# Kernel tuning notes

Hardware: AMD Instinct MI355X
Metric: run time of the kernel (lower is better)

## Reference

```python
import jax, jax.numpy as jnp
import numpy as np

BN_EPS = 1e-5

def _sqdist(a, b):
    # a: (B,N,3), b: (B,M,3) -> (B,N,M)
    return (jnp.sum(a**2, -1)[:, :, None] + jnp.sum(b**2, -1)[:, None, :]
            - 2.0 * jnp.einsum('bnc,bmc->bnm', a, b))

def _knn_idx(pts, k):
    # smallest-k neighbor indices, (B,N,k)
    d = _sqdist(pts, pts)
    _, idx = jax.lax.top_k(-d, k)
    return idx

def _group(feat, idx):
    # feat (B,C,N), idx (B,N,K) -> (B,C,N,K)
    return jax.vmap(lambda f, i: f[:, i])(feat, idx)

def _gather_pts(pts, idx):
    # pts (B,M,C), idx (B,...) -> (B,...,C)
    return jax.vmap(lambda p, i: p[i])(pts, idx)

def _conv1(w, b, x):
    # 1x1 conv1d: w (O,C), x (B,C,N)
    return jnp.einsum('oc,bcn->bon', w, x) + b[None, :, None]

def _conv2(w, x, b=None):
    # 1x1 conv2d: w (O,C), x (B,C,N,K)
    y = jnp.einsum('oc,bcnk->bonk', w, x)
    return y if b is None else y + b[None, :, None, None]

def _bn_eval(x, gamma, beta):
    # eval-mode BatchNorm2d with running_mean=0, running_var=1
    s = gamma / jnp.sqrt(1.0 + BN_EPS)
    return x * s[None, :, None, None] + beta[None, :, None, None]

def _lgrp(x_q, x, P_anchor, map_idx, anchor_dist, lw1, lw2, lw3, k=16):
    # x_q, x: (B,n,3) -> weights (B,dim,n,k)
    d = _sqdist(x_q, x)
    _, idx = jax.lax.top_k(-d, k)                      # (B,n,k)
    neighbors = _gather_pts(x, idx)                    # (B,n,k,3)
    R1 = jnp.abs(x_q[:, :, None, :] - neighbors)       # (B,n,k,3)
    B_idx = _gather_pts(map_idx[..., None], idx)[..., 0]  # (B,n,k)
    anchorA = _gather_pts(P_anchor, map_idx)           # (B,n,3)
    anchorB = _gather_pts(P_anchor, B_idx)             # (B,n,k,3)
    dA = jnp.linalg.norm(x_q - anchorA, axis=-1)       # (B,n)
    dB = jnp.linalg.norm(neighbors - anchorB, axis=-1) # (B,n,k)
    dAB = jax.vmap(lambda ad, a, bi: ad[a[:, None], bi])(anchor_dist, map_idx, B_idx)
    R2s = dA[:, :, None] + dAB + dB                    # (B,n,k)
    R2 = jnp.broadcast_to(R2s[..., None], R1.shape)
    feats = jnp.concatenate([R1, R2], axis=-1).transpose(0, 3, 1, 2)  # (B,6,n,k)
    h = jax.nn.relu(_conv2(lw1, feats))
    h = jax.nn.relu(_conv2(lw2, h))
    return _conv2(lw3, h)                              # (B,dim,n,k)

def setup_inputs() -> dict:
    key = jax.random.key(0)
    ks = jax.random.split(key, 32)
    B, C_in, n, dim, M, k = 2, 128, 2048, 256, 128, 16
    hid_p, hid_a = 64, dim * 4
    s = 0.05
    inp = {
        'x': jax.random.normal(ks[0], (B, C_in, n), jnp.float32),
        'pos': jax.random.normal(ks[1], (B, 3, n), jnp.float32),
        'fps_idx': jax.random.randint(ks[2], (B, n), 0, n),
        'P_anchor': jax.random.normal(ks[3], (B, M, 3), jnp.float32),
        'map_idx': jax.random.randint(ks[4], (B, n), 0, M),
        'anchor_dist': jax.random.uniform(ks[5], (B, M, M), jnp.float32) * 2.0,
        'w_start': jax.random.normal(ks[6], (dim, C_in)) * s,
        'b_start': jnp.zeros((dim,), jnp.float32),
        'w_key': jax.random.normal(ks[7], (dim, dim)) * s,
        'b_key': jnp.zeros((dim,), jnp.float32),
        'w_query': jax.random.normal(ks[8], (dim, dim)) * s,
        'b_query': jnp.zeros((dim,), jnp.float32),
        'w_value': jax.random.normal(ks[9], (dim, dim)) * s,
        'b_value': jnp.zeros((dim,), jnp.float32),
        'pw1': jax.random.normal(ks[10], (hid_p, 3)) * s,
        'pb1': jnp.zeros((hid_p,), jnp.float32),
        'pg1': jnp.ones((hid_p,), jnp.float32),
        'pbt1': jnp.zeros((hid_p,), jnp.float32),
        'pw2': jax.random.normal(ks[11], (dim, hid_p)) * s,
        'pb2': jnp.zeros((dim,), jnp.float32),
        'lw1': jax.random.normal(ks[12], (32, 6)) * s,
        'lw2': jax.random.normal(ks[13], (64, 32)) * s,
        'lw3': jax.random.normal(ks[14], (dim, 64)) * s,
        'aw1': jax.random.normal(ks[15], (hid_a, dim)) * s,
        'ab1': jnp.zeros((hid_a,), jnp.float32),
        'ag1': jnp.ones((hid_a,), jnp.float32),
        'abt1': jnp.zeros((hid_a,), jnp.float32),
        'aw2': jax.random.normal(ks[16], (dim, hid_a)) * s,
        'ab2': jnp.zeros((dim,), jnp.float32),
        'w_end': jax.random.normal(ks[17], (C_in, dim)) * s,
        'b_end': jnp.zeros((C_in,), jnp.float32),
    }
    return inp

def reference(x, pos, fps_idx, P_anchor, map_idx, anchor_dist,
              w_start, b_start, w_key, b_key, w_query, b_query, w_value, b_value,
              pw1, pb1, pg1, pbt1, pw2, pb2, lw1, lw2, lw3,
              aw1, ab1, ag1, abt1, aw2, ab2, w_end, b_end):
    n_knn = 16
    identity = x
    xf = _conv1(w_start, b_start, x)                   # (B,dim,n)
    pos_f = pos.transpose(0, 2, 1)                     # (B,n,3)
    idx_knn = _knn_idx(pos_f, n_knn)                   # (B,n,k)
    key_f = _conv1(w_key, b_key, xf)
    value = _conv1(w_value, b_value, xf)
    query = _conv1(w_query, b_query, xf)
    key_g = _group(key_f, idx_knn)                     # (B,dim,n,k)
    qk_rel = query[:, :, :, None] - key_g
    pos_rel = pos[:, :, :, None] - _group(pos, idx_knn)
    f_l = _lgrp(pos_f, pos_f, P_anchor, map_idx, anchor_dist, lw1, lw2, lw3, k=16)
    # pos_mlp: conv-bn-relu-conv
    h = _bn_eval(_conv2(pw1, pos_rel, pb1), pg1, pbt1)
    pos_emb = _conv2(pw2, jax.nn.relu(h), pb2)         # (B,dim,n,k)
    # attn_mlp
    a = _bn_eval(_conv2(aw1, qk_rel + pos_emb + f_l, ab1), ag1, abt1)
    attention = _conv2(aw2, jax.nn.relu(a), ab2)
    attention = jax.nn.softmax(attention, axis=-1)
    value_e = value[:, :, :, None] + pos_emb + f_l
    agg = jnp.sum(attention * value_e, axis=-1)        # (B,dim,n)
    y = _conv1(w_end, b_end, agg)
    return y + identity
```

## Files before the change

kernel.cpp:

```cpp
#include <hip/hip_runtime.h>
#include <hip/hip_bf16.h>

typedef __hip_bfloat16 bf16;
typedef unsigned short u16;
typedef __attribute__((ext_vector_type(8))) short s8v;
typedef __attribute__((ext_vector_type(4))) float f32x4;

#define NP    2048
#define DC    256
#define MA    128
#define KNN_  16
#define LKV   768

#define MFMA_B16(a,b,c) __builtin_amdgcn_mfma_f32_16x16x32_bf16(a,b,c,0,0,0)

__device__ __forceinline__ float u2f(u16 u){ return __uint_as_float(((unsigned int)u)<<16); }
__device__ __forceinline__ u16 f2u(float f){ bf16 h=__float2bfloat16(f); u16 us; __builtin_memcpy(&us,&h,2); return us; }

__device__ __forceinline__ s8v ldpk(const u16* pk, int rb, int KS, int ks, int l){
  return *(const s8v*)(pk + (((size_t)((rb*KS + ks)*64 + l))<<3));
}
__device__ __forceinline__ s8v ldsB(const u16* base, int col, int k0, int rshift){
  int byte = ((col<<rshift) + (k0<<1)) ^ ((col&7)<<4);
  return *(const s8v*)((const char*)base + byte);
}
__device__ __forceinline__ void st2(u16* base, int col, int ch0, int rshift,
                                    float v0, float v1, float v2, float v3){
  uint2 pkv;
  pkv.x = (unsigned)f2u(v0) | ((unsigned)f2u(v1)<<16);
  pkv.y = (unsigned)f2u(v2) | ((unsigned)f2u(v3)<<16);
  int byte = ((col<<rshift) + (ch0<<1)) ^ ((col&7)<<4);
  *(uint2*)((char*)base + byte) = pkv;
}
__device__ __forceinline__ void st1(u16* base, int col, int ch, int rshift, float v){
  int byte = ((col<<rshift) + (ch<<1)) ^ ((col&7)<<4);
  *(u16*)((char*)base + byte) = f2u(v);
}
__device__ __forceinline__ void ld4s(const u16* base, int col, int ch0, int rshift, float* o){
  int byte = ((col<<rshift) + (ch0<<1)) ^ ((col&7)<<4);
  uint2 pkv = *(const uint2*)((const char*)base + byte);
  o[0] = u2f(pkv.x & 0xffff); o[1] = u2f(pkv.x>>16);
  o[2] = u2f(pkv.y & 0xffff); o[3] = u2f(pkv.y>>16);
}

template<bool XT, bool OT, bool RES>
__global__ __launch_bounds__(256) void mgemm(
    const u16* __restrict__ apk, const float* __restrict__ X,
    const float* __restrict__ bias, const float* __restrict__ resid,
    float* __restrict__ out, int M, int N, int K, int ldo)
{
  __shared__ u16 Bt[64*256];
  const int tid = threadIdx.x;
  const int w = tid>>6, l = tid&63, k = l&15, g = l>>4;
  const int n0 = blockIdx.x*64, m0 = blockIdx.y*128, bb = blockIdx.z;
  const int KS = K >> 5;
  if constexpr (!XT) {
    for (int e = tid*4; e < 64*K; e += 1024) {
      int kk = e >> 6, c = e & 63;
      float4 v = *(const float4*)(X + (size_t)bb*K*N + (size_t)kk*N + n0 + c);
      st1(Bt, c+0, kk, 9, v.x); st1(Bt, c+1, kk, 9, v.y);
      st1(Bt, c+2, kk, 9, v.z); st1(Bt, c+3, kk, 9, v.w);
    }
  } else {
    for (int e = tid*4; e < 64*256; e += 1024) {
      int c = e >> 8, kk = e & 255;
      float4 v = *(const float4*)(X + ((size_t)bb*N + n0 + c)*256 + kk);
      st2(Bt, c, kk, 9, v.x, v.y, v.z, v.w);
    }
  }
  __syncthreads();
  f32x4 acc[2][4] = {};
  const int rbase = (m0>>4) + w*2;
  for (int ks = 0; ks < KS; ks++) {
    s8v a0 = ldpk(apk, rbase,   KS, ks, l);
    s8v a1 = ldpk(apk, rbase+1, KS, ks, l);
#pragma unroll
    for (int cf = 0; cf < 4; cf++) {
      s8v bF = ldsB(Bt, cf*16 + k, ks*32 + g*8, 9);
      acc[0][cf] = MFMA_B16(a0, bF, acc[0][cf]);
      acc[1][cf] = MFMA_B16(a1, bF, acc[1][cf]);
    }
  }
#pragma unroll
  for (int ri = 0; ri < 2; ri++) {
    int mrow = m0 + w*32 + ri*16 + g*4;
#pragma unroll
    for (int r = 0; r < 4; r++) {
      int m = mrow + r;
      float bv = bias[m];
#pragma unroll
      for (int cf = 0; cf < 4; cf++) {
        int n = n0 + cf*16 + k;
        float v = acc[ri][cf][r] + bv;
        if constexpr (RES) v += resid[((size_t)bb*M + m)*N + n];
        if constexpr (OT) out[((size_t)bb*N + n)*ldo + m] = v;
        else              out[((size_t)bb*M + m)*N + n] = v;
      }
    }
  }
}

__global__ __launch_bounds__(1024) void knn_kernel(const float* __restrict__ pos, int* __restrict__ idx)
{
  __shared__ float px[NP], py[NP], pz[NP], pn[NP];
  const int tid = threadIdx.x;
  const int w = tid >> 6, l = tid & 63;
  const int bb = blockIdx.x >> 7;
  const int q0 = (blockIdx.x & 127) * 16;
  const float* pp = pos + (size_t)bb * 3 * NP;
  for (int t = tid; t < NP; t += 1024) {
    float x = pp[t], y = pp[NP + t], z = pp[2*NP + t];
    px[t] = x; py[t] = y; pz[t] = z; pn[t] = x*x + y*y + z*z;
  }
  __syncthreads();
  const int qi = q0 + w;
  const float qx = px[qi], qy = py[qi], qz = pz[qi], qn = pn[qi];
  float bd[16]; int bi[16];
#pragma unroll
  for (int t = 0; t < 16; t++) { bd[t] = 3.4e38f; bi[t] = -1; }
  float worst = 3.4e38f;
  for (int t = 0; t < 32; t++) {
    int j = t*64 + l;
    float d = qn + pn[j] - 2.f * (qx*px[j] + qy*py[j] + qz*pz[j]);
    if (__any(d < worst)) {
      float cd = (d < worst) ? d : 3.4e38f;
      int   cj = j;
#pragma unroll
      for (int s = 0; s < 16; s++) {
        bool sw = cd < bd[s];
        float od = bd[s]; int oj = bi[s];
        bd[s] = sw ? cd : od;  bi[s] = sw ? cj : oj;
        cd    = sw ? od : cd;  cj    = sw ? oj : cj;
      }
      worst = bd[15];
    }
  }
  int myj = 0;
#pragma unroll
  for (int r = 0; r < 16; r++) {
    float md = bd[0]; int mj = bi[0];
#pragma unroll
    for (int o = 1; o < 64; o <<= 1) {
      float od = __shfl_xor(md, o);
      int   oj = __shfl_xor(mj, o);
      bool tk = (od < md) || (od == md && ((unsigned)oj < (unsigned)mj));
      md = tk ? od : md;  mj = tk ? oj : mj;
    }
    if (l == r) myj = mj;
    bool win = (bi[0] == mj);
#pragma unroll
    for (int s = 0; s < 15; s++) {
      bd[s] = win ? bd[s+1] : bd[s];
      bi[s] = win ? bi[s+1] : bi[s];
    }
    bd[15] = win ? 3.4e38f : bd[15];
  }
  if (l < 16) idx[((size_t)bb * NP + qi) * KNN_ + l] = myj;
}

__global__ __launch_bounds__(256) void prep_kernel(
    const float* __restrict__ aw1, const float* __restrict__ aw2,
    const float* __restrict__ lw3, const float* __restrict__ pw2,
    const float* __restrict__ w_start, const float* __restrict__ w_key,
    const float* __restrict__ w_query, const float* __restrict__ w_value,
    const float* __restrict__ w_end,
    const float* __restrict__ b_key, const float* __restrict__ b_query,
    const float* __restrict__ b_value,
    const float* __restrict__ ag1, const float* __restrict__ ab1, const float* __restrict__ abt1,
    const float* __restrict__ pg1, const float* __restrict__ pb1, const float* __restrict__ pbt1,
    u16* __restrict__ aw1pk, u16* __restrict__ aw2pk, u16* __restrict__ wppk,
    u16* __restrict__ wstpk, u16* __restrict__ wkqvpk, u16* __restrict__ wendpk,
    float* __restrict__ sa, float* __restrict__ oa, float* __restrict__ sp,
    float* __restrict__ op_, float* __restrict__ bkqv)
{
  int i = blockIdx.x * 256 + threadIdx.x;
  const float inv = rsqrtf(1.0f + 1e-5f);
  if (i < 262144) {
    int rb = i >> 12, rem = i & 4095, ks = rem >> 9, l = (rem >> 3) & 63, j = rem & 7;
    int row = rb*16 + (l & 15), colk = ks*32 + (l >> 4)*8 + j;
    aw1pk[i] = f2u(aw1[(size_t)row*256 + colk]); return;
  }
  i -= 262144;
  if (i < 262144) {
    int rb = i >> 14, rem = i & 16383, ks = rem >> 9, l = (rem >> 3) & 63, j = rem & 7;
    int row = rb*16 + (l & 15), colk = ks*32 + (l >> 4)*8 + j;
    aw2pk[i] = f2u(aw2[(size_t)row*1024 + colk]); return;
  }
  i -= 262144;
  if (i < 32768) {
    int rb = i >> 11, rem = i & 2047, ks = rem >> 9, l = (rem >> 3) & 63, j = rem & 7;
    int row = rb*16 + (l & 15), colk = ks*32 + (l >> 4)*8 + j;
    float v = (colk < 64) ? lw3[row*64 + colk] : pw2[row*64 + (colk - 64)];
    wppk[i] = f2u(v); return;
  }
  i -= 32768;
  if (i < 32768) {
    int rb = i >> 11, rem = i & 2047, ks = rem >> 9, l = (rem >> 3) & 63, j = rem & 7;
    int row = rb*16 + (l & 15), colk = ks*32 + (l >> 4)*8 + j;
    wstpk[i] = f2u(w_start[(size_t)row*128 + colk]); return;
  }
  i -= 32768;
  if (i < 196608) {
    int rb = i >> 12, rem = i & 4095, ks = rem >> 9, l = (rem >> 3) & 63, j = rem & 7;
    int row = rb*16 + (l & 15), colk = ks*32 + (l >> 4)*8 + j;
    float v = (row < 256) ? w_key[(size_t)row*256 + colk]
            : (row < 512) ? w_query[(size_t)(row-256)*256 + colk]
                          : w_value[(size_t)(row-512)*256 + colk];
    wkqvpk[i] = f2u(v); return;
  }
  i -= 196608;
  if (i < 32768) {
    int rb = i >> 12, rem = i & 4095, ks = rem >> 9, l = (rem >> 3) & 63, j = rem & 7;
    int row = rb*16 + (l & 15), colk = ks*32 + (l >> 4)*8 + j;
    wendpk[i] = f2u(w_end[(size_t)row*256 + colk]); return;
  }
  i -= 32768;
  if (i < 1024) { float s_ = ag1[i]*inv; sa[i] = s_; oa[i] = ab1[i]*s_ + abt1[i]; return; }
  i -= 1024;
  if (i < 64)  { float s_ = pg1[i]*inv; sp[i] = s_; op_[i] = pb1[i]*s_ + pbt1[i]; return; }
  i -= 64;
  if (i < 768) {
    bkqv[i] = (i < 256) ? b_key[i] : (i < 512) ? b_query[i-256] : b_value[i-512];
  }
}

__global__ __launch_bounds__(256, 2) void fused_attn(
    const float* __restrict__ kqv, const int* __restrict__ knn_idx,
    const float* __restrict__ pos, const int* __restrict__ map_idx,
    const float* __restrict__ P_anchor, const float* __restrict__ adist,
    const float* __restrict__ lw1f, const float* __restrict__ lw2f, const float* __restrict__ pw1f,
    const float* __restrict__ spv, const float* __restrict__ opv, const float* __restrict__ pb2f,
    const u16* __restrict__ aw1pk, const float* __restrict__ sav, const float* __restrict__ oav,
    const u16* __restrict__ aw2pk, const u16* __restrict__ wppk, const float* __restrict__ ab2f,
    float* __restrict__ aggT)
{
  __shared__ __align__(16) char smem[40960];
  u16*   s_t   = (u16*)smem;
  u16*   hid_t = (u16*)(smem + 32768);
  float* fFEAT = (float*)smem;
  float* fPREL = (float*)(smem + 1632);
  u16*   fH1   = (u16*) (smem + 2448);

  const int tid = threadIdx.x;
  const int w = tid >> 6, l = tid & 63;
  const int k = l & 15, g = l >> 4;
  const int p0 = blockIdx.x * 4;
  const int b = p0 >> 11, pi0 = p0 & 2047;
  const int pi = pi0 + w;
  const int col_w = w*16 + k;

  const float* kqvB = kqv + (size_t)b * NP * LKV;
  const int* knnB = knn_idx + ((size_t)b * NP) * KNN_;

  if (l < 16) {
    int kk = l;
    int j = knnB[(size_t)pi * KNN_ + kk];
    const float* pp = pos + (size_t)b * 3 * NP;
    float qx = pp[pi], qy = pp[NP+pi], qz = pp[2*NP+pi];
    float nx = pp[j],  ny = pp[NP+j],  nz = pp[2*NP+j];
    float r1x = qx-nx, r1y = qy-ny, r1z = qz-nz;
    fPREL[(w*3+0)*17+kk] = r1x; fPREL[(w*3+1)*17+kk] = r1y; fPREL[(w*3+2)*17+kk] = r1z;
    int mi = map_idx[b*NP + pi];
    int bj = map_idx[b*NP + j];
    const float* pa = P_anchor + (size_t)b * MA * 3;
    float ax = pa[mi*3], ay = pa[mi*3+1], az = pa[mi*3+2];
    float bx = pa[bj*3], by = pa[bj*3+1], bz = pa[bj*3+2];
    float dA = sqrtf((qx-ax)*(qx-ax)+(qy-ay)*(qy-ay)+(qz-az)*(qz-az));
    float dB = sqrtf((nx-bx)*(nx-bx)+(ny-by)*(ny-by)+(nz-bz)*(nz-bz));
    float dAB = adist[(size_t)b*MA*MA + mi*MA + bj];
    float r2 = dA + dAB + dB;
    fFEAT[(w*6+0)*17+kk] = fabsf(r1x); fFEAT[(w*6+1)*17+kk] = fabsf(r1y);
    fFEAT[(w*6+2)*17+kk] = fabsf(r1z);
    fFEAT[(w*6+3)*17+kk] = r2; fFEAT[(w*6+4)*17+kk] = r2; fFEAT[(w*6+5)*17+kk] = r2;
  }
  __syncthreads();

  {
    float f0=fFEAT[(w*6+0)*17+k], f1=fFEAT[(w*6+1)*17+k], f2=fFEAT[(w*6+2)*17+k],
          f3=fFEAT[(w*6+3)*17+k], f4=fFEAT[(w*6+4)*17+k], f5=fFEAT[(w*6+5)*17+k];
#pragma unroll
    for (int jj = 0; jj < 8; jj++) {
      int h = g*8 + jj;
      const float* wp = lw1f + h*6;
      float v = wp[0]*f0 + wp[1]*f1 + wp[2]*f2 + wp[3]*f3 + wp[4]*f4 + wp[5]*f5;
      fH1[(w*32+h)*17+k] = f2u(fmaxf(v, 0.f));
    }
  }
  __syncthreads();

  {
    float hr[32];
#pragma unroll
    for (int t = 0; t < 32; t++) hr[t] = u2f(fH1[(w*32+t)*17+k]);
#pragma unroll
    for (int jj = 0; jj < 16; jj++) {
      int h = g*16 + jj;
      const float4* wp = (const float4*)(lw2f + h*32);
      float a = 0.f;
#pragma unroll
      for (int t4 = 0; t4 < 8; t4++) {
        float4 wv = wp[t4];
        a += wv.x*hr[t4*4] + wv.y*hr[t4*4+1] + wv.z*hr[t4*4+2] + wv.w*hr[t4*4+3];
      }
      st1(hid_t, col_w, h, 7, fmaxf(a, 0.f));
    }
  }
  __syncthreads();

  f32x4 accs[4][4];
  {
#pragma unroll
    for (int fr = 0; fr < 4; fr++) {
      int ch0 = w*64 + fr*16 + g*4;
      const float4 p4 = *(const float4*)(pb2f + ch0);
#pragma unroll
      for (int fc = 0; fc < 4; fc++) {
        int j = knnB[(size_t)(pi0 + fc) * KNN_ + k];
        const float4 q4 = *(const float4*)(kqvB + (size_t)(pi0 + fc)*LKV + 256 + ch0);
        const float4 k4 = *(const float4*)(kqvB + (size_t)j*LKV + ch0);
        accs[fr][fc][0] = q4.x - k4.x + p4.x;
        accs[fr][fc][1] = q4.y - k4.y + p4.y;
        accs[fr][fc][2] = q4.z - k4.z + p4.z;
        accs[fr][fc][3] = q4.w - k4.w + p4.w;
      }
    }
#pragma unroll
    for (int ks = 0; ks < 2; ks++) {
      s8v aF[4];
#pragma unroll
      for (int fr = 0; fr < 4; fr++) aF[fr] = ldpk(wppk, w*4 + fr, 4, ks, l);
#pragma unroll
      for (int fc = 0; fc < 4; fc++) {
        s8v bF = ldsB(hid_t, fc*16 + k, ks*32 + g*8, 7);
#pragma unroll
        for (int fr = 0; fr < 4; fr++) accs[fr][fc] = MFMA_B16(aF[fr], bF, accs[fr][fc]);
      }
    }
  }
  __syncthreads();

  {
    float pr0 = fPREL[(w*3+0)*17+k], pr1 = fPREL[(w*3+1)*17+k], pr2 = fPREL[(w*3+2)*17+k];
#pragma unroll
    for (int jj = 0; jj < 16; jj++) {
      int h = g*16 + jj;
      float d = pw1f[h*3]*pr0 + pw1f[h*3+1]*pr1 + pw1f[h*3+2]*pr2;
      st1(hid_t, col_w, h, 7, fmaxf(d*spv[h] + opv[h], 0.f));
    }
  }
  __syncthreads();

  {
#pragma unroll
    for (int ks = 0; ks < 2; ks++) {
      s8v aF[4];
#pragma unroll
      for (int fr = 0; fr < 4; fr++) aF[fr] = ldpk(wppk, w*4 + fr, 4, 2 + ks, l);
#pragma unroll
      for (int fc = 0; fc < 4; fc++) {
        s8v bF = ldsB(hid_t, fc*16 + k, ks*32 + g*8, 7);
#pragma unroll
        for (int fr = 0; fr < 4; fr++) accs[fr][fc] = MFMA_B16(aF[fr], bF, accs[fr][fc]);
      }
    }
#pragma unroll
    for (int fr = 0; fr < 4; fr++)
#pragma unroll
      for (int fc = 0; fc < 4; fc++)
        st2(s_t, fc*16 + k, w*64 + fr*16 + g*4, 9,
            accs[fr][fc][0], accs[fr][fc][1], accs[fr][fc][2], accs[fr][fc][3]);
  }
  __syncthreads();

  f32x4 acc2[4][4];
#pragma unroll
  for (int fr = 0; fr < 4; fr++) {
    const float4 a4 = *(const float4*)(ab2f + w*64 + fr*16 + g*4);
#pragma unroll
    for (int fc = 0; fc < 4; fc++) {
      acc2[fr][fc][0] = a4.x; acc2[fr][fc][1] = a4.y;
      acc2[fr][fc][2] = a4.z; acc2[fr][fc][3] = a4.w;
    }
  }

  for (int c = 0; c < 16; c++) {
    f32x4 acc1[4] = {};
    const int rb = c*4 + w;
#pragma unroll
    for (int ks = 0; ks < 8; ks++) {
      s8v a0 = ldpk(aw1pk, rb, 8, ks, l);
#pragma unroll
      for (int cf = 0; cf < 4; cf++) {
        s8v bF = ldsB(s_t, cf*16 + k, ks*32 + g*8, 9);
        acc1[cf] = MFMA_B16(a0, bF, acc1[cf]);
      }
    }
    __syncthreads();
    {
      int hl = w*16 + g*4;
      int hg = rb*16 + g*4;
      const float4 sc = *(const float4*)(sav + hg);
      const float4 of = *(const float4*)(oav + hg);
#pragma unroll
      for (int cf = 0; cf < 4; cf++) {
        float v0 = fmaxf(acc1[cf][0]*sc.x + of.x, 0.f);
        float v1 = fmaxf(acc1[cf][1]*sc.y + of.y, 0.f);
        float v2 = fmaxf(acc1[cf][2]*sc.z + of.z, 0.f);
        float v3 = fmaxf(acc1[cf][3]*sc.w + of.w, 0.f);
        st2(hid_t, cf*16 + k, hl, 7, v0, v1, v2, v3);
      }
    }
    __syncthreads();
#pragma unroll
    for (int ks = 0; ks < 2; ks++) {
      s8v aF[4];
#pragma unroll
      for (int rf = 0; rf < 4; rf++) aF[rf] = ldpk(aw2pk, w*4 + rf, 32, c*2 + ks, l);
#pragma unroll
      for (int cf = 0; cf < 4; cf++) {
        s8v bF = ldsB(hid_t, cf*16 + k, ks*32 + g*8, 7);
#pragma unroll
        for (int rf = 0; rf < 4; rf++) acc2[rf][cf] = MFMA_B16(aF[rf], bF, acc2[rf][cf]);
      }
    }
  }

#pragma unroll
  for (int fc = 0; fc < 4; fc++) {
    int j = knnB[(size_t)(pi0 + fc) * KNN_ + k];
    const float* qp = kqvB + (size_t)(pi0 + fc)*LKV + 256;
    const float* kp = kqvB + (size_t)j*LKV;
    const float* vp = kqvB + (size_t)(pi0 + fc)*LKV + 512;
#pragma unroll
    for (int fr = 0; fr < 4; fr++) {
      int ch0 = w*64 + fr*16 + g*4;
      float q4[4], k4[4], v4[4], s4[4], res[4];
      *(float4*)q4 = *(const float4*)(qp + ch0);
      *(float4*)k4 = *(const float4*)(kp + ch0);
      *(float4*)v4 = *(const float4*)(vp + ch0);
      ld4s(s_t, fc*16 + k, ch0, 9, s4);
#pragma unroll
      for (int r = 0; r < 4; r++) {
        float a = acc2[fr][fc][r];
        float m = a;
        m = fmaxf(m, __shfl_xor(m, 1, 16)); m = fmaxf(m, __shfl_xor(m, 2, 16));
        m = fmaxf(m, __shfl_xor(m, 4, 16)); m = fmaxf(m, __shfl_xor(m, 8, 16));
        float ex = __expf(a - m);
        float se = ex;
        se += __shfl_xor(se, 1, 16); se += __shfl_xor(se, 2, 16);
        se += __shfl_xor(se, 4, 16); se += __shfl_xor(se, 8, 16);
        float watt = ex / se;
        float ve = v4[r] - q4[r] + k4[r] + s4[r];
        float cc = watt * ve;
        cc += __shfl_xor(cc, 1, 16); cc += __shfl_xor(cc, 2, 16);
        cc += __shfl_xor(cc, 4, 16); cc += __shfl_xor(cc, 8, 16);
        res[r] = cc;
      }
      if (k == 0)
        *(float4*)(aggT + ((size_t)(b*NP) + pi0 + fc)*DC + ch0) =
            make_float4(res[0], res[1], res[2], res[3]);
    }
  }
}

extern "C" void kernel_launch(void* const* d_in, const int* in_sizes, int n_in,
                              void* d_out, int out_size, void* d_ws, size_t ws_size,
                              hipStream_t stream)
{
  const float* x        = (const float*)d_in[0];
  const float* pos      = (const float*)d_in[1];
  const float* P_anchor = (const float*)d_in[3];
  const int*   map_idx  = (const int*)  d_in[4];
  const float* adist    = (const float*)d_in[5];
  const float* w_start  = (const float*)d_in[6];
  const float* b_start  = (const float*)d_in[7];
  const float* w_key    = (const float*)d_in[8];
  const float* b_key    = (const float*)d_in[9];
  const float* w_query  = (const float*)d_in[10];
  const float* b_query  = (const float*)d_in[11];
  const float* w_value  = (const float*)d_in[12];
  const float* b_value  = (const float*)d_in[13];
  const float* pw1      = (const float*)d_in[14];
  const float* pb1      = (const float*)d_in[15];
  const float* pg1      = (const float*)d_in[16];
  const float* pbt1     = (const float*)d_in[17];
  const float* pw2      = (const float*)d_in[18];
  const float* pb2      = (const float*)d_in[19];
  const float* lw1      = (const float*)d_in[20];
  const float* lw2      = (const float*)d_in[21];
  const float* lw3      = (const float*)d_in[22];
  const float* aw1      = (const float*)d_in[23];
  const float* ab1      = (const float*)d_in[24];
  const float* ag1      = (const float*)d_in[25];
  const float* abt1     = (const float*)d_in[26];
  const float* aw2      = (const float*)d_in[27];
  const float* ab2      = (const float*)d_in[28];
  const float* w_end    = (const float*)d_in[29];
  const float* b_end    = (const float*)d_in[30];

  if (ws_size < (size_t)4672384 * 4) return;

  float* ws     = (float*)d_ws;
  float* xf     = ws + 0;
  float* aggT   = ws + 0;
  float* kqvT   = ws + 1048576;
  u16*   aw1pk  = (u16*)(ws + 4194304);
  u16*   aw2pk  = (u16*)(ws + 4325376);
  u16*   wppk   = (u16*)(ws + 4456448);
  u16*   wstpk  = (u16*)(ws + 4472832);
  u16*   wkqvpk = (u16*)(ws + 4489216);
  u16*   wendpk = (u16*)(ws + 4587520);
  float* sa     = ws + 4603904;
  float* oa     = ws + 4604928;
  float* sp     = ws + 4605952;
  float* op_    = ws + 4606016;
  float* bkqv   = ws + 4606080;
  int*   knn_i  = (int*)(ws + 4606848);

  prep_kernel<<<3208, 256, 0, stream>>>(aw1, aw2, lw3, pw2,
      w_start, w_key, w_query, w_value, w_end, b_key, b_query, b_value,
      ag1, ab1, abt1, pg1, pb1, pbt1,
      aw1pk, aw2pk, wppk, wstpk, wkqvpk, wendpk, sa, oa, sp, op_, bkqv);

  mgemm<false, false, false><<<dim3(32, 2, 2), 256, 0, stream>>>(
      wstpk, x, b_start, nullptr, xf, 256, NP, 128, 0);

  knn_kernel<<<256, 1024, 0, stream>>>(pos, knn_i);

  mgemm<false, true, false><<<dim3(32, 6, 2), 256, 0, stream>>>(
      wkqvpk, xf, bkqv, nullptr, kqvT, 768, NP, 256, LKV);

  fused_attn<<<1024, 256, 0, stream>>>(kqvT, knn_i,
      pos, map_idx, P_anchor, adist,
      lw1, lw2, pw1, sp, op_, pb2,
      aw1pk, sa, oa, aw2pk, wppk, ab2, aggT);

  mgemm<true, false, true><<<dim3(32, 1, 2), 256, 0, stream>>>(
      wendpk, aggT, b_end, x, (float*)d_out, 128, NP, 256, 0);
}
```

Measured before the change: 234.8 us.

## Use 8 waves per block in fused attention, halving per-wave channel tiles

The fused attention kernel now runs 512 threads (8 waves) per block instead of 256. Each wave owns 32 output channels instead of 64, which halves the per-wave MFMA accumulator arrays. The lw2 and pos_mlp hidden computations now run in one phase and write into a single 128-wide hidden buffer, so the two pos_emb GEMM passes merge into one K=128 pass. This targets more latency hiding and lower register pressure per wave. The costs are more LDS per block (48KB), an extra barrier, and the larger block must still fit within the new launch bounds.

```diff
diff --git a/kernel.cpp b/kernel.cpp
--- a/kernel.cpp
+++ b/kernel.cpp
@@ -224,7 +224,7 @@
   }
 }
 
-__global__ __launch_bounds__(256, 2) void fused_attn(
+__global__ __launch_bounds__(512, 4) void fused_attn(
     const float* __restrict__ kqv, const int* __restrict__ knn_idx,
     const float* __restrict__ pos, const int* __restrict__ map_idx,
     const float* __restrict__ P_anchor, const float* __restrict__ adist,
@@ -234,7 +234,7 @@
     const u16* __restrict__ aw2pk, const u16* __restrict__ wppk, const float* __restrict__ ab2f,
     float* __restrict__ aggT)
 {
-  __shared__ __align__(16) char smem[40960];
+  __shared__ __align__(16) char smem[49152];
   u16*   s_t   = (u16*)smem;
   u16*   hid_t = (u16*)(smem + 32768);
   float* fFEAT = (float*)smem;
@@ -246,14 +246,13 @@
   const int k = l & 15, g = l >> 4;
   const int p0 = blockIdx.x * 4;
   const int b = p0 >> 11, pi0 = p0 & 2047;
-  const int pi = pi0 + w;
-  const int col_w = w*16 + k;
 
   const float* kqvB = kqv + (size_t)b * NP * LKV;
   const int* knnB = knn_idx + ((size_t)b * NP) * KNN_;
 
-  if (l < 16) {
+  if (w < 4 && l < 16) {
     int kk = l;
+    int pi = pi0 + w;
     int j = knnB[(size_t)pi * KNN_ + kk];
     const float* pp = pos + (size_t)b * 3 * NP;
     float qx = pp[pi], qy = pp[NP+pi], qz = pp[2*NP+pi];
@@ -275,7 +274,7 @@
   }
   __syncthreads();
 
-  {
+  if (w < 4) {
     float f0=fFEAT[(w*6+0)*17+k], f1=fFEAT[(w*6+1)*17+k], f2=fFEAT[(w*6+2)*17+k],
           f3=fFEAT[(w*6+3)*17+k], f4=fFEAT[(w*6+4)*17+k], f5=fFEAT[(w*6+5)*17+k];
 #pragma unroll
@@ -289,12 +288,14 @@
   __syncthreads();
 
   {
+    const int p = w & 3, hh = w >> 2;
+    const int col_p = p*16 + k;
     float hr[32];
 #pragma unroll
-    for (int t = 0; t < 32; t++) hr[t] = u2f(fH1[(w*32+t)*17+k]);
-#pragma unroll
-    for (int jj = 0; jj < 16; jj++) {
-      int h = g*16 + jj;
+    for (int t = 0; t < 32; t++) hr[t] = u2f(fH1[(p*32+t)*17+k]);
+#pragma unroll
+    for (int jj = 0; jj < 8; jj++) {
+      int h = hh*32 + g*8 + jj;
       const float4* wp = (const float4*)(lw2f + h*32);
       float a = 0.f;
 #pragma unroll
@@ -302,16 +303,23 @@
         float4 wv = wp[t4];
         a += wv.x*hr[t4*4] + wv.y*hr[t4*4+1] + wv.z*hr[t4*4+2] + wv.w*hr[t4*4+3];
       }
-      st1(hid_t, col_w, h, 7, fmaxf(a, 0.f));
+      st1(hid_t, col_p, h, 8, fmaxf(a, 0.f));
+    }
+    float pr0 = fPREL[(p*3+0)*17+k], pr1 = fPREL[(p*3+1)*17+k], pr2 = fPREL[(p*3+2)*17+k];
+#pragma unroll
+    for (int jj = 0; jj < 8; jj++) {
+      int h = hh*32 + g*8 + jj;
+      float d = pw1f[h*3]*pr0 + pw1f[h*3+1]*pr1 + pw1f[h*3+2]*pr2;
+      st1(hid_t, col_p, 64 + h, 8, fmaxf(d*spv[h] + opv[h], 0.f));
     }
   }
   __syncthreads();
 
-  f32x4 accs[4][4];
   {
-#pragma unroll
-    for (int fr = 0; fr < 4; fr++) {
-      int ch0 = w*64 + fr*16 + g*4;
+    f32x4 accs[2][4];
+#pragma unroll
+    for (int fr = 0; fr < 2; fr++) {
+      int ch0 = w*32 + fr*16 + g*4;
       const float4 p4 = *(const float4*)(pb2f + ch0);
 #pragma unroll
       for (int fc = 0; fc < 4; fc++) {
@@ -325,57 +333,30 @@
       }
     }
 #pragma unroll
-    for (int ks = 0; ks < 2; ks++) {
-      s8v aF[4];
-#pragma unroll
-      for (int fr = 0; fr < 4; fr++) aF[fr] = ldpk(wppk, w*4 + fr, 4, ks, l);
+    for (int ks = 0; ks < 4; ks++) {
+      s8v a0 = ldpk(wppk, w*2 + 0, 4, ks, l);
+      s8v a1 = ldpk(wppk, w*2 + 1, 4, ks, l);
 #pragma unroll
       for (int fc = 0; fc < 4; fc++) {
-        s8v bF = ldsB(hid_t, fc*16 + k, ks*32 + g*8, 7);
-#pragma unroll
-        for (int fr = 0; fr < 4; fr++) accs[fr][fc] = MFMA_B16(aF[fr], bF, accs[fr][fc]);
-      }
-    }
+        s8v bF = ldsB(hid_t, fc*16 + k, ks*32 + g*8, 8);
+        accs[0][fc] = MFMA_B16(a0, bF, accs[0][fc]);
+        accs[1][fc] = MFMA_B16(a1, bF, accs[1][fc]);
+      }
+    }
+    __syncthreads();
+#pragma unroll
+    for (int fr = 0; fr < 2; fr++)
+#pragma unroll
+      for (int fc = 0; fc < 4; fc++)
+        st2(s_t, fc*16 + k, w*32 + fr*16 + g*4, 9,
+            accs[fr][fc][0], accs[fr][fc][1], accs[fr][fc][2], accs[fr][fc][3]);
   }
   __syncthreads();
 
-  {
-    float pr0 = fPREL[(w*3+0)*17+k], pr1 = fPREL[(w*3+1)*17+k], pr2 = fPREL[(w*3+2)*17+k];
-#pragma unroll
-    for (int jj = 0; jj < 16; jj++) {
-      int h = g*16 + jj;
-      float d = pw1f[h*3]*pr0 + pw1f[h*3+1]*pr1 + pw1f[h*3+2]*pr2;
-      st1(hid_t, col_w, h, 7, fmaxf(d*spv[h] + opv[h], 0.f));
-    }
-  }
-  __syncthreads();
-
-  {
-#pragma unroll
-    for (int ks = 0; ks < 2; ks++) {
-      s8v aF[4];
-#pragma unroll
-      for (int fr = 0; fr < 4; fr++) aF[fr] = ldpk(wppk, w*4 + fr, 4, 2 + ks, l);
-#pragma unroll
-      for (int fc = 0; fc < 4; fc++) {
-        s8v bF = ldsB(hid_t, fc*16 + k, ks*32 + g*8, 7);
-#pragma unroll
-        for (int fr = 0; fr < 4; fr++) accs[fr][fc] = MFMA_B16(aF[fr], bF, accs[fr][fc]);
-      }
-    }
-#pragma unroll
-    for (int fr = 0; fr < 4; fr++)
-#pragma unroll
-      for (int fc = 0; fc < 4; fc++)
-        st2(s_t, fc*16 + k, w*64 + fr*16 + g*4, 9,
-            accs[fr][fc][0], accs[fr][fc][1], accs[fr][fc][2], accs[fr][fc][3]);
-  }
-  __syncthreads();
-
-  f32x4 acc2[4][4];
-#pragma unroll
-  for (int fr = 0; fr < 4; fr++) {
-    const float4 a4 = *(const float4*)(ab2f + w*64 + fr*16 + g*4);
+  f32x4 acc2[2][4];
+#pragma unroll
+  for (int fr = 0; fr < 2; fr++) {
+    const float4 a4 = *(const float4*)(ab2f + w*32 + fr*16 + g*4);
 #pragma unroll
     for (int fc = 0; fc < 4; fc++) {
       acc2[fr][fc][0] = a4.x; acc2[fr][fc][1] = a4.y;
@@ -383,9 +364,9 @@
     }
   }
 
-  for (int c = 0; c < 16; c++) {
+  for (int c = 0; c < 8; c++) {
     f32x4 acc1[4] = {};
-    const int rb = c*4 + w;
+    const int rb = c*8 + w;
 #pragma unroll
     for (int ks = 0; ks < 8; ks++) {
       s8v a0 = ldpk(aw1pk, rb, 8, ks, l);
@@ -407,20 +388,19 @@
         float v1 = fmaxf(acc1[cf][1]*sc.y + of.y, 0.f);
         float v2 = fmaxf(acc1[cf][2]*sc.z + of.z, 0.f);
         float v3 = fmaxf(acc1[cf][3]*sc.w + of.w, 0.f);
-        st2(hid_t, cf*16 + k, hl, 7, v0, v1, v2, v3);
+        st2(hid_t, cf*16 + k, hl, 8, v0, v1, v2, v3);
       }
     }
     __syncthreads();
 #pragma unroll
-    for (int ks = 0; ks < 2; ks++) {
-      s8v aF[4];
-#pragma unroll
-      for (int rf = 0; rf < 4; rf++) aF[rf] = ldpk(aw2pk, w*4 + rf, 32, c*2 + ks, l);
+    for (int ks = 0; ks < 4; ks++) {
+      s8v a0 = ldpk(aw2pk, w*2 + 0, 32, c*4 + ks, l);
+      s8v a1 = ldpk(aw2pk, w*2 + 1, 32, c*4 + ks, l);
 #pragma unroll
       for (int cf = 0; cf < 4; cf++) {
-        s8v bF = ldsB(hid_t, cf*16 + k, ks*32 + g*8, 7);
-#pragma unroll
-        for (int rf = 0; rf < 4; rf++) acc2[rf][cf] = MFMA_B16(aF[rf], bF, acc2[rf][cf]);
+        s8v bF = ldsB(hid_t, cf*16 + k, ks*32 + g*8, 8);
+        acc2[0][cf] = MFMA_B16(a0, bF, acc2[0][cf]);
+        acc2[1][cf] = MFMA_B16(a1, bF, acc2[1][cf]);
       }
     }
   }
@@ -432,8 +412,8 @@
     const float* kp = kqvB + (size_t)j*LKV;
     const float* vp = kqvB + (size_t)(pi0 + fc)*LKV + 512;
 #pragma unroll
-    for (int fr = 0; fr < 4; fr++) {
-      int ch0 = w*64 + fr*16 + g*4;
+    for (int fr = 0; fr < 2; fr++) {
+      int ch0 = w*32 + fr*16 + g*4;
       float q4[4], k4[4], v4[4], s4[4], res[4];
       *(float4*)q4 = *(const float4*)(qp + ch0);
       *(float4*)k4 = *(const float4*)(kp + ch0);
@@ -530,7 +510,7 @@
   mgemm<false, true, false><<<dim3(32, 6, 2), 256, 0, stream>>>(
       wkqvpk, xf, bkqv, nullptr, kqvT, 768, NP, 256, LKV);
 
-  fused_attn<<<1024, 256, 0, stream>>>(kqvT, knn_i,
+  fused_attn<<<1024, 512, 0, stream>>>(kqvT, knn_i,
       pos, map_idx, P_anchor, adist,
       lw1, lw2, pw1, sp, op_, pb2,
       aw1pk, sa, oa, aw2pk, wppk, ab2, aggT);
```

Result: no change. 235.9 us (+0.5%).
